# Kernel tuning notes

Measured on AMD Instinct MI355X. Metric: run time of the kernel, lower is better.

## Reference

```python
import jax, jax.numpy as jnp
import numpy as np

B, L, D = 4, 2048, 512


def setup_inputs() -> dict:
    key = jax.random.key(0)
    ks = jax.random.split(key, 12)
    f32 = jnp.float32
    mk = lambda k, s: jax.random.normal(k, s, dtype=f32)
    # xavier-uniform-ish init scale for the linear weights
    w_qkv_lim = np.sqrt(6.0 / (6 * D + 6 * D)).astype(np.float32)
    w_out_lim = np.sqrt(6.0 / (2 * D + 2 * D)).astype(np.float32)
    return {
        "q_real": mk(ks[0], (B, L, D)),
        "q_imag": mk(ks[1], (B, L, D)),
        "k_real": mk(ks[2], (B, L, D)),
        "k_imag": mk(ks[3], (B, L, D)),
        "v_real": mk(ks[4], (B, L, D)),
        "v_imag": mk(ks[5], (B, L, D)),
        "pad_mask": jax.random.randint(ks[6], (B, L), 0, 2).astype(jnp.bool_),
        "W_qkv": jax.random.uniform(ks[7], (6 * D, 6 * D), f32, -w_qkv_lim, w_qkv_lim),
        "b_qkv": jnp.zeros((6 * D,), f32),
        "W_out": jax.random.uniform(ks[8], (2 * D, 2 * D), f32, -w_out_lim, w_out_lim),
        "b_out": jnp.zeros((2 * D,), f32),
    }


def reference(q_real, q_imag, k_real, k_imag, v_real, v_imag, pad_mask,
              W_qkv, b_qkv, W_out, b_out):
    b, l, d = q_real.shape
    # fused QKV projection over concatenated real/imag streams: [B, L, 6D]
    x = jnp.concatenate([q_real, q_imag, k_real, k_imag, v_real, v_imag], axis=-1)
    qkv = x @ W_qkv.T + b_qkv                      # torch Linear: x @ W^T + b
    qkv = qkv.reshape(b, l, 6, d)
    q_r, k_r = qkv[:, :, 0], qkv[:, :, 2]
    v_r, v_i = qkv[:, :, 4], qkv[:, :, 5]
    scale = jnp.asarray(d, jnp.float32) ** -0.5
    scores = jnp.einsum('bqd,bkd->bqk', q_r, k_r) * scale   # [B, L, L]
    scores = jnp.where(pad_mask[:, None, :], -jnp.inf, scores)
    attn = jax.nn.softmax(scores, axis=-1)         # dropout omitted (eval mode)
    out_real = jnp.einsum('bqk,bkd->bqd', attn, v_r)
    out_imag = jnp.einsum('bqk,bkd->bqd', attn, v_i)
    out = jnp.concatenate([out_real, out_imag], axis=-1) @ W_out.T + b_out
    return out[..., :d], out[..., d:]
```

## Files before the change

kernel.cpp:

```cpp
#include <hip/hip_runtime.h>
#include <cstdint>
#include <cstddef>

typedef unsigned short ushort;
typedef __attribute__((ext_vector_type(8))) short short8;
typedef __attribute__((ext_vector_type(16))) float f32x16;

__device__ __forceinline__ float bf2f(ushort u) {
  union { unsigned u; float f; } c; c.u = ((unsigned)u) << 16; return c.f;
}
__device__ __forceinline__ ushort f2bf(float f) {
  union { float f; unsigned u; } c; c.f = f;
  unsigned u = c.u;
  return (ushort)((u + 0x7fffu + ((u >> 16) & 1u)) >> 16);
}

#define G2L(g, l) __builtin_amdgcn_global_load_lds( \
    (const __attribute__((address_space(1))) void*)(g), \
    (__attribute__((address_space(3))) void*)(l), 16, 0, 0)

#define BARRIER() do { asm volatile("" ::: "memory"); __builtin_amdgcn_s_barrier(); asm volatile("" ::: "memory"); } while (0)
#define LGKMC(N) do { asm volatile("s_waitcnt lgkmcnt(%0)" :: "n"(N) : "memory"); __builtin_amdgcn_sched_barrier(0); } while (0)

__device__ __forceinline__ unsigned ldsoff(const void* p) {
  return (unsigned)(unsigned long long)(__attribute__((address_space(3))) const void*)p;
}

struct MArgs {
  const ushort* A; int lda; long asz;
  const ushort* B; int ldb; long bsz;
  void* C; int ldc; long csz;
  int K;
  const float* bias;
  float* C2;
};

template<int MODE, int BN>
__launch_bounds__(512, 2)
__global__ void mfma_gemm(MArgs g) {
  constexpr int BM = 256;
  constexpr int WN = BN / 64;
  constexpr int WM = 8 / WN;
  constexpr int WMSZ = BM / WM;
  constexpr int MF = WMSZ / 32;
  constexpr int NBG = BN / 64;
  constexpr int LPS = 4 + NBG;
  constexpr int RD = MF + 2;

  __shared__ __attribute__((aligned(16))) ushort As[2][BM * 64];
  __shared__ __attribute__((aligned(16))) ushort Bs[2][BN * 64];

  const int tid = threadIdx.x;
  const int lane = tid & 63;
  const int wave = tid >> 6;
  const int z = blockIdx.z;

  int bx = blockIdx.x, by = blockIdx.y;
  {
    const int gx = gridDim.x;
    const int nwg = gx * gridDim.y;
    int wg = by * gx + bx;
    wg = (wg & 7) * (nwg >> 3) + (wg >> 3);
    bx = wg % gx; by = wg / gx;
  }
  const long m0 = (long)by * BM;
  const long n0 = (long)bx * BN;
  const ushort* Ab = g.A + (long)z * g.asz;
  const ushort* Bb = g.B + (long)z * g.bsz;

  const int srow = tid >> 3;
  const long skel = (long)((((tid & 7) - srow) & 7) * 8);
  const ushort* ga[4];
  const ushort* gb[NBG];
#pragma unroll
  for (int q = 0; q < 4; ++q) ga[q] = Ab + (m0 + q * 64 + srow) * (long)g.lda + skel;
#pragma unroll
  for (int q = 0; q < NBG; ++q) gb[q] = Bb + (n0 + q * 64 + srow) * (long)g.ldb + skel;

  const int l31 = lane & 31, hb = lane >> 5;
  const int wmi = wave / WN, wni = wave % WN;
  unsigned aoffB[MF]; int arot[MF];
#pragma unroll
  for (int mf = 0; mf < MF; ++mf) {
    const int r = wmi * WMSZ + mf * 32 + l31;
    aoffB[mf] = (unsigned)(r * 128);
    arot[mf] = (r + hb) & 7;
  }
  unsigned boffB[2]; int brot[2];
#pragma unroll
  for (int nf = 0; nf < 2; ++nf) {
    const int r = wni * 64 + nf * 32 + l31;
    boffB[nf] = (unsigned)(r * 128);
    brot[nf] = (r + hb) & 7;
  }

  f32x16 acc[MF][2];
#pragma unroll
  for (int mf = 0; mf < MF; ++mf)
#pragma unroll
    for (int nf = 0; nf < 2; ++nf)
#pragma unroll
      for (int r = 0; r < 16; ++r) acc[mf][nf][r] = 0.f;

  auto STAGEF = [&](int buf, int t) {
    const long ko = (long)t * 64;
#pragma unroll
    for (int q = 0; q < 4; ++q) G2L(ga[q] + ko, &As[buf][q * 4096 + tid * 8]);
#pragma unroll
    for (int q = 0; q < NBG; ++q) G2L(gb[q] + ko, &Bs[buf][q * 4096 + tid * 8]);
  };

  const unsigned abB[2] = { ldsoff(&As[0][0]), ldsoff(&As[1][0]) };
  const unsigned bbB[2] = { ldsoff(&Bs[0][0]), ldsoff(&Bs[1][0]) };
  short8 av[2][MF], bv[2][2];

#define ISSUE_H(s, h, ab, bb) do { \
  _Pragma("unroll") for (int mf = 0; mf < MF; ++mf) { \
    unsigned o = (ab) + aoffB[mf] + (unsigned)((((2 * (h) + arot[mf]) & 7) << 4)); \
    asm volatile("ds_read_b128 %0, %1" : "=v"(av[s][mf]) : "v"(o)); \
  } \
  _Pragma("unroll") for (int nf = 0; nf < 2; ++nf) { \
    unsigned o = (bb) + boffB[nf] + (unsigned)((((2 * (h) + brot[nf]) & 7) << 4)); \
    asm volatile("ds_read_b128 %0, %1" : "=v"(bv[s][nf]) : "v"(o)); \
  } \
} while (0)
#define MFMA_S(s) do { \
  __builtin_amdgcn_s_setprio(1); \
  _Pragma("unroll") for (int mf = 0; mf < MF; ++mf) \
  _Pragma("unroll") for (int nf = 0; nf < 2; ++nf) \
    acc[mf][nf] = __builtin_amdgcn_mfma_f32_32x32x16_bf16(av[s][mf], bv[s][nf], acc[mf][nf], 0, 0, 0); \
  __builtin_amdgcn_s_setprio(0); \
} while (0)

  STAGEF(0, 0);
  STAGEF(1, 1);
  asm volatile("s_waitcnt vmcnt(%0)" :: "n"(LPS) : "memory");
  BARRIER();
  ISSUE_H(0, 0, abB[0], bbB[0]);

  const int nt = g.K >> 6;
  for (int t = 0; t < nt; ++t) {
    const int cur = t & 1;
    const unsigned ab = abB[cur], bb = bbB[cur];

    ISSUE_H(1, 1, ab, bb);
    LGKMC(RD);
    MFMA_S(0);
    ISSUE_H(0, 2, ab, bb);
    LGKMC(RD);
    MFMA_S(1);
    ISSUE_H(1, 3, ab, bb);
    LGKMC(RD);
    MFMA_S(0);
    LGKMC(0);

    if (t + 1 < nt) {
      BARRIER();
      if (t + 2 < nt) {
        STAGEF(cur, t + 2);
        asm volatile("s_waitcnt vmcnt(%0)" :: "n"(LPS) : "memory");
      } else {
        asm volatile("s_waitcnt vmcnt(0)" ::: "memory");
      }
      BARRIER();
      ISSUE_H(0, 0, abB[cur ^ 1], bbB[cur ^ 1]);
    }
    MFMA_S(1);
  }
#undef ISSUE_H
#undef MFMA_S

  const int cc = l31;
  const int rbase = 4 * hb;
  ushort* Cu = (ushort*)g.C + (long)z * g.csz;
  float* Cf = (float*)g.C;
#pragma unroll
  for (int mf = 0; mf < MF; ++mf) {
#pragma unroll
    for (int nf = 0; nf < 2; ++nf) {
      const long col = n0 + wni * 64 + nf * 32 + cc;
      float bsv = 0.f;
      if (MODE == 0 || MODE == 3) bsv = g.bias[col];
#pragma unroll
      for (int r = 0; r < 16; ++r) {
        const long row = m0 + wmi * WMSZ + mf * 32 + (r & 3) + 8 * (r >> 2) + rbase;
        float v = acc[mf][nf][r] + bsv;
        if (MODE == 3) {
          float* dst = (col < 512) ? (Cf + row * 512 + col) : (g.C2 + row * 512 + (col - 512));
          *dst = v;
        } else {
          Cu[row * (long)g.ldc + col] = f2bf(v);
        }
      }
    }
  }
}

__global__ void cvt_x6(const float* x0, const float* x1, const float* x2,
                       const float* x3, const float* x4, const float* x5, ushort* X) {
  const long m = blockIdx.y;
  const int c4 = (blockIdx.x * 256 + threadIdx.x) * 4;
  const int p = c4 >> 9, d = c4 & 511;
  const float* xp;
  switch (p) {
    case 0: xp = x0; break; case 1: xp = x1; break; case 2: xp = x2; break;
    case 3: xp = x3; break; case 4: xp = x4; break; default: xp = x5; break;
  }
  float4 v = *(const float4*)(xp + m * 512 + d);
  ushort4 o; o.x = f2bf(v.x); o.y = f2bf(v.y); o.z = f2bf(v.z); o.w = f2bf(v.w);
  *(ushort4*)(X + m * 3072 + c4) = o;
}

__device__ __forceinline__ int chunk_map(int c) { return (c == 0) ? 0 : (c == 1) ? 2 : (c == 2) ? 4 : 5; }

__global__ void cvt_w4(const float* W, ushort* Wq4) {
  const long r = blockIdx.y;
  const int c4 = (blockIdx.x * 256 + threadIdx.x) * 4;
  const long wr = (long)chunk_map((int)(r >> 9)) * 512 + (r & 511);
  float4 v = *(const float4*)(W + wr * 3072 + c4);
  ushort4 o; o.x = f2bf(v.x); o.y = f2bf(v.y); o.z = f2bf(v.z); o.w = f2bf(v.w);
  *(ushort4*)(Wq4 + r * 3072 + c4) = o;
}

__global__ void cvt_wout(const float* W, ushort* Wo) {
  const long r = blockIdx.y;
  const int c4 = threadIdx.x * 4;
  float4 v = *(const float4*)(W + r * 1024 + c4);
  ushort4 o; o.x = f2bf(v.x); o.y = f2bf(v.y); o.z = f2bf(v.z); o.w = f2bf(v.w);
  *(ushort4*)(Wo + r * 1024 + c4) = o;
}

__global__ void mk_bias4(const float* bqkv, float* b4) {
  const int n = blockIdx.x * 256 + threadIdx.x;
  b4[n] = bqkv[chunk_map(n >> 9) * 512 + (n & 511)];
}

__global__ void transpose_v(const ushort* QKV, ushort* Vt) {
  __shared__ ushort t2[64][68];
  const int tid = threadIdx.x;
  const int k0 = blockIdx.x * 64, n0 = blockIdx.y * 64, b = blockIdx.z;
  const ushort* src = QKV + (long)b * 2048 * 2048 + 1024;
#pragma unroll
  for (int i = 0; i < 2; ++i) {
    const int slot = i * 256 + tid;
    const int kr = slot >> 3, nc = slot & 7;
    short8 v = *(const short8*)(src + (long)(k0 + kr) * 2048 + (n0 + nc * 8));
#pragma unroll
    for (int j = 0; j < 8; ++j) t2[nc * 8 + j][kr] = (ushort)v[j];
  }
  __syncthreads();
  ushort* dst = Vt + (long)b * 1024 * 2048;
#pragma unroll
  for (int i = 0; i < 2; ++i) {
    const int slot = i * 256 + tid;
    const int nr = slot >> 3, kc = slot & 7;
    short8 v;
#pragma unroll
    for (int j = 0; j < 8; ++j) v[j] = (short)t2[nr][kc * 8 + j];
    *(short8*)(dst + (long)(n0 + nr) * 2048 + (k0 + kc * 8)) = v;
  }
}

__launch_bounds__(256)
__global__ void softmax_rows(ushort* S, const int* mask) {
  const int lane = threadIdx.x & 63;
  const int wave = threadIdx.x >> 6;
  const long row = (long)blockIdx.x * 4 + wave;
  const int* m = mask + (row >> 11) * 2048 + lane * 32;
  ushort* s = S + row * 2048 + lane * 32;
  const float scale = 0.04419417382415922f;

  short8 raw[4];
#pragma unroll
  for (int i = 0; i < 4; ++i) raw[i] = *(const short8*)(s + i * 8);
  int4 mi[8];
#pragma unroll
  for (int i = 0; i < 8; ++i) mi[i] = *(const int4*)(m + i * 4);

  float v[32];
  int mk[32];
#pragma unroll
  for (int i = 0; i < 8; ++i) {
    mk[i * 4 + 0] = mi[i].x; mk[i * 4 + 1] = mi[i].y;
    mk[i * 4 + 2] = mi[i].z; mk[i * 4 + 3] = mi[i].w;
  }
#pragma unroll
  for (int i = 0; i < 32; ++i) v[i] = bf2f((ushort)raw[i >> 3][i & 7]) * scale;

  float mx = -INFINITY;
#pragma unroll
  for (int i = 0; i < 32; ++i) if (!mk[i]) mx = fmaxf(mx, v[i]);
#pragma unroll
  for (int off = 32; off; off >>= 1) mx = fmaxf(mx, __shfl_xor(mx, off));

  float sum = 0.f;
#pragma unroll
  for (int i = 0; i < 32; ++i) {
    float e = mk[i] ? 0.f : __expf(v[i] - mx);
    v[i] = e;
    sum += e;
  }
#pragma unroll
  for (int off = 32; off; off >>= 1) sum += __shfl_xor(sum, off);

  float r = 1.f / sum;
  short8 out[4];
#pragma unroll
  for (int i = 0; i < 32; ++i) out[i >> 3][i & 7] = (short)f2bf(v[i] * r);
#pragma unroll
  for (int i = 0; i < 4; ++i) *(short8*)(s + i * 8) = out[i];
}

extern "C" void kernel_launch(void* const* d_in, const int* in_sizes, int n_in,
                              void* d_out, int out_size, void* d_ws, size_t ws_size,
                              hipStream_t stream) {
  const float* qr = (const float*)d_in[0];
  const float* qi = (const float*)d_in[1];
  const float* kr = (const float*)d_in[2];
  const float* ki = (const float*)d_in[3];
  const float* vr = (const float*)d_in[4];
  const float* vi = (const float*)d_in[5];
  const int* pm = (const int*)d_in[6];
  const float* Wqkv = (const float*)d_in[7];
  const float* bqkv = (const float*)d_in[8];
  const float* Wout = (const float*)d_in[9];
  const float* bout = (const float*)d_in[10];
  float* out = (float*)d_out;

  char* base = (char*)d_ws;
  ushort* QKV   = (ushort*)(base);
  ushort* Wq4   = (ushort*)(base + 33554432);
  ushort* Wo    = (ushort*)(base + 46137344);
  float*  b4    = (float*) (base + 48234496);
  char*   uni   = base + 48242688;
  ushort* Xbf   = (ushort*)(uni);
  ushort* Vt    = (ushort*)(uni);
  ushort* S     = (ushort*)(uni + 16777216);
  ushort* AO    = (ushort*)(uni + 50331648);

  cvt_x6<<<dim3(3, 8192), 256, 0, stream>>>(qr, qi, kr, ki, vr, vi, Xbf);
  cvt_w4<<<dim3(3, 2048), 256, 0, stream>>>(Wqkv, Wq4);
  cvt_wout<<<dim3(1, 1024), 256, 0, stream>>>(Wout, Wo);
  mk_bias4<<<8, 256, 0, stream>>>(bqkv, b4);

  {
    MArgs a{};
    a.A = Xbf; a.lda = 3072; a.asz = 0;
    a.B = Wq4; a.ldb = 3072; a.bsz = 0;
    a.C = QKV; a.ldc = 2048; a.csz = 0;
    a.K = 3072; a.bias = b4;
    mfma_gemm<0, 256><<<dim3(8, 32, 1), 512, 0, stream>>>(a);
  }

  transpose_v<<<dim3(32, 16, 4), 256, 0, stream>>>(QKV, Vt);

  {
    MArgs a{};
    a.A = QKV;        a.lda = 2048; a.asz = (long)2048 * 2048;
    a.B = QKV + 512;  a.ldb = 2048; a.bsz = (long)2048 * 2048;
    a.C = S;          a.ldc = 2048; a.csz = (long)2048 * 2048;
    a.K = 512;
    mfma_gemm<1, 256><<<dim3(8, 8, 4), 512, 0, stream>>>(a);
  }

  softmax_rows<<<2048, 256, 0, stream>>>(S, pm);

  {
    MArgs a{};
    a.A = S;  a.lda = 2048; a.asz = (long)2048 * 2048;
    a.B = Vt; a.ldb = 2048; a.bsz = (long)1024 * 2048;
    a.C = AO; a.ldc = 1024; a.csz = (long)2048 * 1024;
    a.K = 2048;
    mfma_gemm<2, 128><<<dim3(8, 8, 4), 512, 0, stream>>>(a);
  }

  {
    MArgs a{};
    a.A = AO; a.lda = 1024; a.asz = 0;
    a.B = Wo; a.ldb = 1024; a.bsz = 0;
    a.C = out; a.ldc = 512; a.csz = 0;
    a.C2 = out + (long)8192 * 512;
    a.K = 1024; a.bias = bout;
    mfma_gemm<3, 128><<<dim3(8, 32, 1), 512, 0, stream>>>(a);
  }
}
```

Measured before the change: 387.9 us.

## Restructure GEMM to 256-thread blocks with fixed BN=128 and K-step of 32

```diff
diff --git a/kernel.cpp b/kernel.cpp
--- a/kernel.cpp
+++ b/kernel.cpp
@@ -35,20 +35,20 @@
   float* C2;
 };
 
-template<int MODE, int BN>
-__launch_bounds__(512, 2)
+template<int MODE, int BM>
+__launch_bounds__(256, 2)
 __global__ void mfma_gemm(MArgs g) {
-  constexpr int BM = 256;
-  constexpr int WN = BN / 64;
-  constexpr int WM = 8 / WN;
-  constexpr int WMSZ = BM / WM;
+  constexpr int BN = 128;
+  constexpr int WMSZ = BM / 2;
   constexpr int MF = WMSZ / 32;
+  constexpr int NF = 2;
+  constexpr int NAG = BM / 64;
   constexpr int NBG = BN / 64;
-  constexpr int LPS = 4 + NBG;
-  constexpr int RD = MF + 2;
-
-  __shared__ __attribute__((aligned(16))) ushort As[2][BM * 64];
-  __shared__ __attribute__((aligned(16))) ushort Bs[2][BN * 64];
+  constexpr int LPS = NAG + NBG;
+  constexpr int RD = MF + NF;
+
+  __shared__ __attribute__((aligned(16))) ushort As[2][BM * 32];
+  __shared__ __attribute__((aligned(16))) ushort Bs[2][BN * 32];
 
   const int tid = threadIdx.x;
   const int lane = tid & 63;
@@ -68,66 +68,68 @@
   const ushort* Ab = g.A + (long)z * g.asz;
   const ushort* Bb = g.B + (long)z * g.bsz;
 
-  const int srow = tid >> 3;
-  const long skel = (long)((((tid & 7) - srow) & 7) * 8);
-  const ushort* ga[4];
+  const int rp = tid >> 3;
+  const int sd = ((tid & 7) - rp) & 7;
+  const int srcrow = rp * 2 + (sd >> 2);
+  const int scol = (sd & 3) * 8;
+  const ushort* ga[NAG];
   const ushort* gb[NBG];
 #pragma unroll
-  for (int q = 0; q < 4; ++q) ga[q] = Ab + (m0 + q * 64 + srow) * (long)g.lda + skel;
-#pragma unroll
-  for (int q = 0; q < NBG; ++q) gb[q] = Bb + (n0 + q * 64 + srow) * (long)g.ldb + skel;
+  for (int q = 0; q < NAG; ++q) ga[q] = Ab + (m0 + q * 64 + srcrow) * (long)g.lda + scol;
+#pragma unroll
+  for (int q = 0; q < NBG; ++q) gb[q] = Bb + (n0 + q * 64 + srcrow) * (long)g.ldb + scol;
 
   const int l31 = lane & 31, hb = lane >> 5;
-  const int wmi = wave / WN, wni = wave % WN;
+  const int wmi = wave >> 1, wni = wave & 1;
   unsigned aoffB[MF]; int arot[MF];
 #pragma unroll
   for (int mf = 0; mf < MF; ++mf) {
     const int r = wmi * WMSZ + mf * 32 + l31;
-    aoffB[mf] = (unsigned)(r * 128);
-    arot[mf] = (r + hb) & 7;
-  }
-  unsigned boffB[2]; int brot[2];
-#pragma unroll
-  for (int nf = 0; nf < 2; ++nf) {
+    aoffB[mf] = (unsigned)((r >> 1) * 128);
+    arot[mf] = ((r & 1) * 4 + hb + ((r >> 1) & 7));
+  }
+  unsigned boffB[NF]; int brot[NF];
+#pragma unroll
+  for (int nf = 0; nf < NF; ++nf) {
     const int r = wni * 64 + nf * 32 + l31;
-    boffB[nf] = (unsigned)(r * 128);
-    brot[nf] = (r + hb) & 7;
-  }
-
-  f32x16 acc[MF][2];
+    boffB[nf] = (unsigned)((r >> 1) * 128);
+    brot[nf] = ((r & 1) * 4 + hb + ((r >> 1) & 7));
+  }
+
+  f32x16 acc[MF][NF];
 #pragma unroll
   for (int mf = 0; mf < MF; ++mf)
 #pragma unroll
-    for (int nf = 0; nf < 2; ++nf)
+    for (int nf = 0; nf < NF; ++nf)
 #pragma unroll
       for (int r = 0; r < 16; ++r) acc[mf][nf][r] = 0.f;
 
   auto STAGEF = [&](int buf, int t) {
-    const long ko = (long)t * 64;
-#pragma unroll
-    for (int q = 0; q < 4; ++q) G2L(ga[q] + ko, &As[buf][q * 4096 + tid * 8]);
-#pragma unroll
-    for (int q = 0; q < NBG; ++q) G2L(gb[q] + ko, &Bs[buf][q * 4096 + tid * 8]);
+    const long ko = (long)t * 32;
+#pragma unroll
+    for (int q = 0; q < NAG; ++q) G2L(ga[q] + ko, &As[buf][q * 2048 + tid * 8]);
+#pragma unroll
+    for (int q = 0; q < NBG; ++q) G2L(gb[q] + ko, &Bs[buf][q * 2048 + tid * 8]);
   };
 
   const unsigned abB[2] = { ldsoff(&As[0][0]), ldsoff(&As[1][0]) };
   const unsigned bbB[2] = { ldsoff(&Bs[0][0]), ldsoff(&Bs[1][0]) };
-  short8 av[2][MF], bv[2][2];
+  short8 av[2][MF], bv[2][NF];
 
 #define ISSUE_H(s, h, ab, bb) do { \
   _Pragma("unroll") for (int mf = 0; mf < MF; ++mf) { \
-    unsigned o = (ab) + aoffB[mf] + (unsigned)((((2 * (h) + arot[mf]) & 7) << 4)); \
+    unsigned o = (ab) + aoffB[mf] + (unsigned)(((2 * (h) + arot[mf]) & 7) << 4); \
     asm volatile("ds_read_b128 %0, %1" : "=v"(av[s][mf]) : "v"(o)); \
   } \
-  _Pragma("unroll") for (int nf = 0; nf < 2; ++nf) { \
-    unsigned o = (bb) + boffB[nf] + (unsigned)((((2 * (h) + brot[nf]) & 7) << 4)); \
+  _Pragma("unroll") for (int nf = 0; nf < NF; ++nf) { \
+    unsigned o = (bb) + boffB[nf] + (unsigned)(((2 * (h) + brot[nf]) & 7) << 4); \
     asm volatile("ds_read_b128 %0, %1" : "=v"(bv[s][nf]) : "v"(o)); \
   } \
 } while (0)
 #define MFMA_S(s) do { \
   __builtin_amdgcn_s_setprio(1); \
   _Pragma("unroll") for (int mf = 0; mf < MF; ++mf) \
-  _Pragma("unroll") for (int nf = 0; nf < 2; ++nf) \
+  _Pragma("unroll") for (int nf = 0; nf < NF; ++nf) \
     acc[mf][nf] = __builtin_amdgcn_mfma_f32_32x32x16_bf16(av[s][mf], bv[s][nf], acc[mf][nf], 0, 0, 0); \
   __builtin_amdgcn_s_setprio(0); \
 } while (0)
@@ -138,18 +140,12 @@
   BARRIER();
   ISSUE_H(0, 0, abB[0], bbB[0]);
 
-  const int nt = g.K >> 6;
+  const int nt = g.K >> 5;
   for (int t = 0; t < nt; ++t) {
     const int cur = t & 1;
     const unsigned ab = abB[cur], bb = bbB[cur];
 
     ISSUE_H(1, 1, ab, bb);
-    LGKMC(RD);
-    MFMA_S(0);
-    ISSUE_H(0, 2, ab, bb);
-    LGKMC(RD);
-    MFMA_S(1);
-    ISSUE_H(1, 3, ab, bb);
     LGKMC(RD);
     MFMA_S(0);
     LGKMC(0);
@@ -177,7 +173,7 @@
 #pragma unroll
   for (int mf = 0; mf < MF; ++mf) {
 #pragma unroll
-    for (int nf = 0; nf < 2; ++nf) {
+    for (int nf = 0; nf < NF; ++nf) {
       const long col = n0 + wni * 64 + nf * 32 + cc;
       float bsv = 0.f;
       if (MODE == 0 || MODE == 3) bsv = g.bias[col];
@@ -349,7 +345,7 @@
     a.B = Wq4; a.ldb = 3072; a.bsz = 0;
     a.C = QKV; a.ldc = 2048; a.csz = 0;
     a.K = 3072; a.bias = b4;
-    mfma_gemm<0, 256><<<dim3(8, 32, 1), 512, 0, stream>>>(a);
+    mfma_gemm<0, 256><<<dim3(16, 32, 1), 256, 0, stream>>>(a);
   }
 
   transpose_v<<<dim3(32, 16, 4), 256, 0, stream>>>(QKV, Vt);
@@ -360,7 +356,7 @@
     a.B = QKV + 512;  a.ldb = 2048; a.bsz = (long)2048 * 2048;
     a.C = S;          a.ldc = 2048; a.csz = (long)2048 * 2048;
     a.K = 512;
-    mfma_gemm<1, 256><<<dim3(8, 8, 4), 512, 0, stream>>>(a);
+    mfma_gemm<1, 256><<<dim3(16, 8, 4), 256, 0, stream>>>(a);
   }
 
   softmax_rows<<<2048, 256, 0, stream>>>(S, pm);
@@ -371,7 +367,7 @@
     a.B = Vt; a.ldb = 2048; a.bsz = (long)1024 * 2048;
     a.C = AO; a.ldc = 1024; a.csz = (long)2048 * 1024;
     a.K = 2048;
-    mfma_gemm<2, 128><<<dim3(8, 8, 4), 512, 0, stream>>>(a);
+    mfma_gemm<2, 128><<<dim3(8, 16, 4), 256, 0, stream>>>(a);
   }
 
   {
@@ -381,6 +377,6 @@
     a.C = out; a.ldc = 512; a.csz = 0;
     a.C2 = out + (long)8192 * 512;
     a.K = 1024; a.bias = bout;
-    mfma_gemm<3, 128><<<dim3(8, 32, 1), 512, 0, stream>>>(a);
-  }
-}
+    mfma_gemm<3, 128><<<dim3(8, 64, 1), 256, 0, stream>>>(a);
+  }
+}
```

After: 422.3 us. +8.9%, slower.
